# Kernel tuning notes

Hardware: AMD Instinct MI355X
Metric: run time of the kernel (lower is better)

Reference implementation:

```python
import jax, jax.numpy as jnp
import numpy as np

N = 100000
E = 1600000
IN_C, HID_C, OUT_C = 128, 64, 40


def setup_inputs() -> dict:
    key = jax.random.key(0)
    ks = jax.random.split(key, 9)
    x = jax.random.normal(ks[0], (N, IN_C), dtype=jnp.float32)
    src = jax.random.randint(ks[1], (E,), 0, N, dtype=jnp.int64)
    dst = jax.random.randint(ks[2], (E,), 0, N, dtype=jnp.int64)
    edge_index = jnp.stack([src, dst], axis=0)
    def glorot(k, fan_in, fan_out):
        s = jnp.sqrt(6.0 / (fan_in + fan_out)).astype(jnp.float32)
        return jax.random.uniform(k, (fan_in, fan_out), jnp.float32, -s, s)
    return {
        "x": x,
        "edge_index": edge_index,
        "W1": glorot(ks[3], IN_C, HID_C), "b1": jnp.zeros((HID_C,), jnp.float32),
        "W2": glorot(ks[4], HID_C, HID_C), "b2": jnp.zeros((HID_C,), jnp.float32),
        "W3": glorot(ks[5], HID_C, OUT_C), "b3": jnp.zeros((OUT_C,), jnp.float32),
    }


def _gcn_norm(edge_index, n_nodes):
    # add self-loops, then symmetric normalization D^-1/2 (A+I) D^-1/2
    loops = jnp.arange(n_nodes, dtype=edge_index.dtype)
    src = jnp.concatenate([edge_index[0], loops])
    dst = jnp.concatenate([edge_index[1], loops])
    deg = jax.ops.segment_sum(jnp.ones_like(dst, dtype=jnp.float32), dst,
                              num_segments=n_nodes)
    dinv = jnp.where(deg > 0, jax.lax.rsqrt(deg), 0.0)
    norm = dinv[src] * dinv[dst]  # [E + N]
    return src, dst, norm


def _gcn_conv(h, W, b, src, dst, norm, n_nodes):
    h = h @ W                                   # [N, out]
    msg = norm[:, None] * h[src]                # gather + scale, [E+N, out]
    out = jax.ops.segment_sum(msg, dst, num_segments=n_nodes)  # scatter-add
    return out + b


def reference(x, edge_index, W1, b1, W2, b2, W3, b3):
    n_nodes = x.shape[0]
    src, dst, norm = _gcn_norm(edge_index, n_nodes)
    h = jax.nn.relu(_gcn_conv(x, W1, b1, src, dst, norm, n_nodes))
    # dropout(p=0.5) is identity in eval mode
    h = jax.nn.relu(_gcn_conv(h, W2, b2, src, dst, norm, n_nodes))
    out = _gcn_conv(h, W3, b3, src, dst, norm, n_nodes)
    return out
```

## Files before the change

kernel.cpp:

```cpp
#include <hip/hip_runtime.h>

#define N_NODES 100000
#define N_EDGES 1600000
#define NBUCK 196
#define BCAP 9600
#define CH 4096
#define NCHUNK ((N_EDGES + CH - 1) / CH)

typedef __attribute__((ext_vector_type(2))) _Float16 half2v;
typedef __attribute__((ext_vector_type(4))) _Float16 half4v;
typedef __attribute__((ext_vector_type(8))) _Float16 half8v;
typedef __attribute__((ext_vector_type(4))) float f32x4;

__device__ __forceinline__ float4 loadX4(const float* X, size_t idx) {
    return *(const float4*)(X + idx);
}
__device__ __forceinline__ float4 loadX4(const _Float16* X, size_t idx) {
    half4v h = *(const half4v*)(X + idx);
    return make_float4((float)h.x, (float)h.y, (float)h.z, (float)h.w);
}


__global__ __launch_bounds__(256) void zero_small(int* p, int n) {
    int i = blockIdx.x * blockDim.x + threadIdx.x;
    if (i < n) p[i] = 0;
}

__global__ __launch_bounds__(256) void multisplit(const int* __restrict__ src,
                                                  const int* __restrict__ dst,
                                                  int* cursor,
                                                  int* __restrict__ bucketed, int e) {
    __shared__ int cnt[NBUCK];
    __shared__ int basel[NBUCK];
    const int t = threadIdx.x;
    const int base_e = blockIdx.x * CH;

    int myS[16], myD[16];
    for (int i = t; i < NBUCK; i += 256) cnt[i] = 0;
    __syncthreads();

#pragma unroll
    for (int k = 0; k < 16; ++k) {
        int i = base_e + k * 256 + t;
        if (i < e) {
            myS[k] = src[i];
            myD[k] = dst[i];
            atomicAdd(&cnt[myD[k] >> 9], 1);
        } else {
            myD[k] = -1;
        }
    }
    __syncthreads();
    for (int i = t; i < NBUCK; i += 256) basel[i] = atomicAdd(&cursor[i], cnt[i]);
    __syncthreads();
    for (int i = t; i < NBUCK; i += 256) cnt[i] = 0;
    __syncthreads();

#pragma unroll
    for (int k = 0; k < 16; ++k) {
        if (myD[k] >= 0) {
            int b = myD[k] >> 9;
            int pos = basel[b] + atomicAdd(&cnt[b], 1);
            if (pos < BCAP)
                bucketed[(size_t)b * BCAP + pos] = ((myD[k] & 511) << 17) | myS[k];
        }
    }
}

__global__ __launch_bounds__(256) void bucket_scan(const int* __restrict__ cursor,
                                                   int* __restrict__ gbase) {
    __shared__ int sm[256];
    const int t = threadIdx.x;
    int v = (t < NBUCK) ? cursor[t] : 0;
    sm[t] = v;
    __syncthreads();
    for (int off = 1; off < 256; off <<= 1) {
        int u = (t >= off) ? sm[t - off] : 0;
        __syncthreads();
        sm[t] += u;
        __syncthreads();
    }
    if (t < NBUCK) gbase[t] = sm[t] - v;
    if (t == NBUCK - 1) gbase[NBUCK] = sm[t];
}

__global__ __launch_bounds__(512) void build_csr(const int* __restrict__ bucketed,
                                                 const int* __restrict__ gbase,
                                                 int* __restrict__ row_ptr,
                                                 float* __restrict__ dinv,
                                                 int* __restrict__ csr_src, int n) {
    __shared__ int vals[BCAP];
    __shared__ int cnt[512];
    __shared__ int lcur[512];
    const int b = blockIdx.x;
    const int t = threadIdx.x;
    const int nb0 = b * 512;
    const int nn = min(512, n - nb0);
    const int gb = gbase[b];
    const int m = gbase[b + 1] - gb;

    cnt[t] = 0;
    __syncthreads();
    for (int i = t; i < m; i += 512) {
        int v = bucketed[(size_t)b * BCAP + i];
        vals[i] = v;
        atomicAdd(&cnt[v >> 17], 1);
    }
    __syncthreads();

    int deg = cnt[t];
    for (int off = 1; off < 512; off <<= 1) {
        int u = (t >= off) ? cnt[t - off] : 0;
        __syncthreads();
        cnt[t] += u;
        __syncthreads();
    }
    int offv = cnt[t] - deg;
    __syncthreads();
    cnt[t] = offv;
    lcur[t] = 0;
    if (t < nn) {
        row_ptr[nb0 + t] = gb + offv;
        dinv[nb0 + t] = rsqrtf((float)(deg + 1));
    }
    if (b == NBUCK - 1 && t == 0) row_ptr[n] = gb + m;
    __syncthreads();

    for (int i = t; i < m; i += 512) {
        int v = vals[i];
        int node = v >> 17;
        int pos = atomicAdd(&lcur[node], 1);
        csr_src[gb + cnt[node] + pos] = v & 0x1FFFF;
    }
}


template <int K>
__global__ __launch_bounds__(256) void transpose_w(const float* __restrict__ W,
                                                   _Float16* __restrict__ Wt) {
    int i = blockIdx.x * 256 + threadIdx.x;
    if (i < K * 64) {
        int k = i >> 6, nn = i & 63;
        Wt[(size_t)nn * K + k] = (_Float16)W[i];
    }
}


__device__ __forceinline__ void stageX_rows(const float* X, _Float16* Xl, int t,
                                            int row0, int n, int K, int SP) {
    for (int i = t; i < 64 * K / 4; i += 256) {
        int r = i / (K / 4), c = (i % (K / 4)) * 4;
        int grow = min(row0 + r, n - 1);
        float4 v = *(const float4*)(X + (size_t)grow * K + c);
        half4v h = {(_Float16)v.x, (_Float16)v.y, (_Float16)v.z, (_Float16)v.w};
        *(half4v*)(Xl + r * SP + c) = h;
    }
}
__device__ __forceinline__ void stageX_rows(const _Float16* X, _Float16* Xl, int t,
                                            int row0, int n, int K, int SP) {
    for (int i = t; i < 64 * K / 8; i += 256) {
        int r = i / (K / 8), c = (i % (K / 8)) * 8;
        int grow = min(row0 + r, n - 1);
        *(half8v*)(Xl + r * SP + c) = *(const half8v*)(X + (size_t)grow * K + c);
    }
}

template <int K, typename XT>
__global__ __launch_bounds__(256) void gemm_mfma64(const XT* __restrict__ X,
                                                   const _Float16* __restrict__ Wt,
                                                   const float* __restrict__ dinv,
                                                   _Float16* __restrict__ Y, int n) {
    constexpr int SP = K + 8;
    __shared__ _Float16 Xl[64 * SP];
    __shared__ _Float16 Wl[64 * SP];
    const int t = threadIdx.x;
    const int wave = t >> 6, lane = t & 63;
    const int row0 = blockIdx.x * 64;
    const int m = lane & 15, quad = lane >> 4;

    for (int i = t; i < 64 * K / 8; i += 256) {
        int r = i / (K / 8), c = (i % (K / 8)) * 8;
        *(half8v*)(Wl + r * SP + c) = *(const half8v*)(Wt + (size_t)r * K + c);
    }
    stageX_rows(X, Xl, t, row0, n, K, SP);
    __syncthreads();

    f32x4 acc[4] = {{0,0,0,0},{0,0,0,0},{0,0,0,0},{0,0,0,0}};
#pragma unroll
    for (int k0 = 0; k0 < K; k0 += 32) {
        half8v a = *(const half8v*)(Xl + (wave * 16 + m) * SP + k0 + quad * 8);
#pragma unroll
        for (int ct = 0; ct < 4; ++ct) {
            half8v b = *(const half8v*)(Wl + (ct * 16 + m) * SP + k0 + quad * 8);
            acc[ct] = __builtin_amdgcn_mfma_f32_16x16x32_f16(a, b, acc[ct], 0, 0, 0);
        }
    }

    float dv[4];
#pragma unroll
    for (int r = 0; r < 4; ++r) {
        int row = row0 + wave * 16 + quad * 4 + r;
        dv[r] = dinv[min(row, n - 1)];
    }
#pragma unroll
    for (int ct = 0; ct < 4; ++ct) {
#pragma unroll
        for (int r = 0; r < 4; ++r) {
            int row = row0 + wave * 16 + quad * 4 + r;
            if (row < n)
                Y[(size_t)row * 64 + ct * 16 + m] = (_Float16)(dv[r] * acc[ct][r]);
        }
    }
}


template <int K, int COUT, typename XT>
__global__ __launch_bounds__(256) void gemm_rt(const XT* __restrict__ X,
                                               const float* __restrict__ W,
                                               const float* __restrict__ dinv,
                                               _Float16* __restrict__ Y, int n) {
    constexpr int KC = 64;
    constexpr int S = KC + 4;
    constexpr int NCH = K / KC;
    __shared__ float Xl[64 * S];
    __shared__ float Wl[KC * COUT];

    const int t = threadIdx.x;
    const int row0 = blockIdx.x * 64;
    const int cg = (t & 15) * 4;
    const int rg = (t >> 4) * 4;

    float acc[4][4] = {};

#pragma unroll
    for (int ch = 0; ch < NCH; ++ch) {
        const int k0 = ch * KC;
        for (int i = t; i < 64 * KC / 4; i += 256) {
            int r = i >> 4;
            int k = (i & 15) * 4;
            int grow = min(row0 + r, n - 1);
            *(float4*)(Xl + r * S + k) = loadX4(X, (size_t)grow * K + k0 + k);
        }
        for (int i = t; i < KC * COUT / 4; i += 256) {
            *(float4*)(Wl + i * 4) = *(const float4*)(W + (size_t)k0 * COUT + (size_t)i * 4);
        }
        __syncthreads();

        if (cg < COUT) {
#pragma unroll 4
            for (int k = 0; k < KC; ++k) {
                float4 w = *(const float4*)(Wl + k * COUT + cg);
                float x0 = Xl[(rg + 0) * S + k];
                float x1 = Xl[(rg + 1) * S + k];
                float x2 = Xl[(rg + 2) * S + k];
                float x3 = Xl[(rg + 3) * S + k];
                acc[0][0] += x0 * w.x; acc[0][1] += x0 * w.y; acc[0][2] += x0 * w.z; acc[0][3] += x0 * w.w;
                acc[1][0] += x1 * w.x; acc[1][1] += x1 * w.y; acc[1][2] += x1 * w.z; acc[1][3] += x1 * w.w;
                acc[2][0] += x2 * w.x; acc[2][1] += x2 * w.y; acc[2][2] += x2 * w.z; acc[2][3] += x2 * w.w;
                acc[3][0] += x3 * w.x; acc[3][1] += x3 * w.y; acc[3][2] += x3 * w.z; acc[3][3] += x3 * w.w;
            }
        }
        __syncthreads();
    }

    if (cg < COUT) {
#pragma unroll
        for (int r = 0; r < 4; ++r) {
            int row = row0 + rg + r;
            if (row < n) {
                float d = dinv[row];
                half4v o = { (_Float16)(d * acc[r][0]), (_Float16)(d * acc[r][1]),
                             (_Float16)(d * acc[r][2]), (_Float16)(d * acc[r][3]) };
                *(half4v*)(Y + (size_t)row * COUT + cg) = o;
            }
        }
    }
}


template <bool RELU>
__global__ __launch_bounds__(256) void aggregate64b(const _Float16* __restrict__ tS,
                                                    const int* __restrict__ row_ptr,
                                                    const int* __restrict__ csr_src,
                                                    const float* __restrict__ dinv,
                                                    const float* __restrict__ bias,
                                                    _Float16* __restrict__ out, int n) {
    const int lane = threadIdx.x & 63;
    const int node = blockIdx.x * 4 + (threadIdx.x >> 6);
    if (node >= n) return;
    const int g = lane >> 3;
    const int c8 = lane & 7;
    const half8v* tS8 = (const half8v*)tS;

    const int beg = row_ptr[node];
    const int cnt = row_ptr[node + 1] - beg;

    half8v accA, accB;
#pragma unroll
    for (int i = 0; i < 8; ++i) { accA[i] = (_Float16)0; accB[i] = (_Float16)0; }

    for (int j0 = 0; j0 < cnt; j0 += 64) {
        const int m = min(64, cnt - j0);
        int sj = csr_src[beg + j0 + min(lane, m - 1)];

        int j = 0;
        for (; j + 16 <= m; j += 16) {
            int e0 = __shfl(sj, j + g);
            int e1 = __shfl(sj, j + 8 + g);
            half8v v0 = tS8[(size_t)e0 * 8 + c8];
            half8v v1 = tS8[(size_t)e1 * 8 + c8];
            accA += v0;
            accB += v1;
        }
        for (; j + 8 <= m; j += 8) {
            int e0 = __shfl(sj, j + g);
            accA += tS8[(size_t)e0 * 8 + c8];
        }
        if (j < m) {
            int idx = j + g;
            int e0 = __shfl(sj, min(idx, m - 1));
            half8v v = tS8[(size_t)e0 * 8 + c8];
            if (idx < m) accB += v;
        }
    }

    float acc[8];
#pragma unroll
    for (int i = 0; i < 8; ++i) acc[i] = (float)accA[i] + (float)accB[i];
#pragma unroll
    for (int off = 8; off < 64; off <<= 1) {
#pragma unroll
        for (int i = 0; i < 8; ++i) acc[i] += __shfl_xor(acc[i], off);
    }

    if (lane < 8) {
        half8v selfh = tS8[(size_t)node * 8 + c8];
        float4 b0 = *(const float4*)(bias + c8 * 8);
        float4 b1 = *(const float4*)(bias + c8 * 8 + 4);
        const float bb[8] = {b0.x, b0.y, b0.z, b0.w, b1.x, b1.y, b1.z, b1.w};
        float d = dinv[node];
        half8v o;
#pragma unroll
        for (int i = 0; i < 8; ++i) {
            float v = bb[i] + d * (acc[i] + (float)selfh[i]);
            if (RELU) v = fmaxf(v, 0.0f);
            o[i] = (_Float16)v;
        }
        ((half8v*)out)[(size_t)node * 8 + c8] = o;
    }
}


__global__ __launch_bounds__(256) void aggregate40v(const _Float16* __restrict__ tS,
                                                    const int* __restrict__ row_ptr,
                                                    const int* __restrict__ csr_src,
                                                    const float* __restrict__ dinv,
                                                    const float* __restrict__ bias,
                                                    float* __restrict__ out, int n) {
    const int lane = threadIdx.x & 63;
    const int node = blockIdx.x * 4 + (threadIdx.x >> 6);
    if (node >= n) return;
    const int g = lane / 20;
    const int c2 = lane - 20 * g;
    const bool act = (g < 3);
    const half2v* tS2 = (const half2v*)tS;

    const int beg = row_ptr[node];
    const int cnt = row_ptr[node + 1] - beg;

    half2v a0 = {(_Float16)0, (_Float16)0}, a1 = a0, a2 = a0, a3 = a0;

    for (int j0 = 0; j0 < cnt; j0 += 64) {
        const int m = min(64, cnt - j0);
        int sj = (lane < m) ? csr_src[beg + j0 + lane] : 0;

        int j = 0;
        for (; j + 12 <= m; j += 12) {
            int i0 = j + g, i1 = j + 3 + g, i2 = j + 6 + g, i3 = j + 9 + g;
            int e0 = __shfl(sj, i0 < m ? i0 : 0);
            int e1 = __shfl(sj, i1 < m ? i1 : 0);
            int e2 = __shfl(sj, i2 < m ? i2 : 0);
            int e3 = __shfl(sj, i3 < m ? i3 : 0);
            half2v v0 = tS2[(size_t)e0 * 20 + c2];
            half2v v1 = tS2[(size_t)e1 * 20 + c2];
            half2v v2 = tS2[(size_t)e2 * 20 + c2];
            half2v v3 = tS2[(size_t)e3 * 20 + c2];
            if (act) { a0 += v0; a1 += v1; a2 += v2; a3 += v3; }
        }
        for (; j + 3 <= m; j += 3) {
            int i0 = j + g;
            int e0 = __shfl(sj, i0 < m ? i0 : 0);
            half2v v0 = tS2[(size_t)e0 * 20 + c2];
            if (act) a0 += v0;
        }
        if (j < m) {
            int idx = j + g;
            int e0 = __shfl(sj, idx < m ? idx : m - 1);
            half2v v = tS2[(size_t)e0 * 20 + c2];
            if (act && idx < m) a1 += v;
        }
    }

    float2 s;
    s.x = ((float)a0.x + (float)a1.x) + ((float)a2.x + (float)a3.x);
    s.y = ((float)a0.y + (float)a1.y) + ((float)a2.y + (float)a3.y);
    float sx1 = __shfl(s.x, lane + 20), sy1 = __shfl(s.y, lane + 20);
    float sx2 = __shfl(s.x, lane + 40), sy2 = __shfl(s.y, lane + 40);
    if (lane < 20) {
        s.x += sx1 + sx2;
        s.y += sy1 + sy2;
        half2v selfh = tS2[(size_t)node * 20 + c2];
        float2 b = ((const float2*)bias)[c2];
        float d = dinv[node];
        float2 o;
        o.x = b.x + d * (s.x + (float)selfh.x);
        o.y = b.y + d * (s.y + (float)selfh.y);
        ((float2*)out)[(size_t)node * 20 + c2] = o;
    }
}


extern "C" void kernel_launch(void* const* d_in, const int* in_sizes, int n_in,
                              void* d_out, int out_size, void* d_ws, size_t ws_size,
                              hipStream_t stream) {
    const float* x  = (const float*)d_in[0];
    const int*   ei = (const int*)d_in[1];
    const int*   src = ei;
    const int*   dst = ei + N_EDGES;
    const float* W1 = (const float*)d_in[2];
    const float* b1 = (const float*)d_in[3];
    const float* W2 = (const float*)d_in[4];
    const float* b2 = (const float*)d_in[5];
    const float* W3 = (const float*)d_in[6];
    const float* b3 = (const float*)d_in[7];
    float* out = (float*)d_out;

    const int N = N_NODES, E = N_EDGES;

    char* p = (char*)d_ws;
    int*   cursor   = (int*)p;              p += 256 * 4;
    int*   gbase    = (int*)p;              p += 256 * 4;
    float* dinv     = (float*)p;            p += (size_t)N * 4;
    int*   row_ptr  = (int*)p;              p += (size_t)(N + 4) * 4;
    int*   bucketed = (int*)p;              p += (size_t)NBUCK * BCAP * 4;
    int*   csr_src  = (int*)p;              p += (size_t)E * 4;
    p = (char*)(((size_t)p + 15) & ~(size_t)15);
    _Float16* Wt1   = (_Float16*)p;         p += (size_t)64 * 128 * 2;
    _Float16* Wt2   = (_Float16*)p;         p += (size_t)64 * 64 * 2;
    _Float16* bufA  = (_Float16*)p;         p += (size_t)N * 64 * 2;
    p = (char*)(((size_t)p + 15) & ~(size_t)15);
    _Float16* bufB  = (_Float16*)p;         p += (size_t)N * 64 * 2;

    zero_small<<<1, 256, 0, stream>>>(cursor, NBUCK);
    transpose_w<128><<<32, 256, 0, stream>>>(W1, Wt1);
    transpose_w<64><<<16, 256, 0, stream>>>(W2, Wt2);
    multisplit<<<NCHUNK, 256, 0, stream>>>(src, dst, cursor, bucketed, E);
    bucket_scan<<<1, 256, 0, stream>>>(cursor, gbase);
    build_csr<<<NBUCK, 512, 0, stream>>>(bucketed, gbase, row_ptr, dinv, csr_src, N);

    const int aggGrid = (N + 3) / 4;
    const int gemmGrid = (N + 63) / 64;

    gemm_mfma64<128, float><<<gemmGrid, 256, 0, stream>>>(x, Wt1, dinv, bufA, N);
    aggregate64b<true><<<aggGrid, 256, 0, stream>>>(bufA, row_ptr, csr_src, dinv, b1, bufB, N);

    gemm_mfma64<64, _Float16><<<gemmGrid, 256, 0, stream>>>(bufB, Wt2, dinv, bufA, N);
    aggregate64b<true><<<aggGrid, 256, 0, stream>>>(bufA, row_ptr, csr_src, dinv, b2, bufB, N);

    gemm_rt<64, 40, _Float16><<<gemmGrid, 256, 0, stream>>>(bufB, W3, dinv, bufA, N);
    aggregate40v<<<aggGrid, 256, 0, stream>>>(bufA, row_ptr, csr_src, dinv, b3, out, N);
}
```

Baseline: 327.5 us.

## Assign one node per 8-lane group in aggregation and pad with a zero row

Both aggregation kernels are reworked so several nodes share a wavefront: 8 lanes per node for the 64-channel layers, and 10 lanes per node with 6 nodes per wave for the 40-channel layer. This replaces the one-wave-per-node scheme, which needed a cross-lane reduction and left most lanes idle on low-degree nodes. Out-of-range neighbor slots are redirected to an extra zeroed row at index n, which the GEMM kernels now write, so the gather loop needs no branches. In exchange, every node in a wave iterates up to the wave's largest degree, which costs work under degree skew. The 64-channel grid of N/32 assumes N is divisible by 32.

Result: faster. 311.3 us (-4.9%).

```diff
diff --git a/kernel.cpp b/kernel.cpp
--- a/kernel.cpp
+++ b/kernel.cpp
@@ -177,6 +177,8 @@
     const int wave = t >> 6, lane = t & 63;
     const int row0 = blockIdx.x * 64;
     const int m = lane & 15, quad = lane >> 4;
+
+    if (blockIdx.x == 0 && t < 32) ((int*)(Y + (size_t)n * 64))[t] = 0;
 
     for (int i = t; i < 64 * K / 8; i += 256) {
         int r = i / (K / 8), c = (i % (K / 8)) * 8;
@@ -229,6 +231,8 @@
     const int row0 = blockIdx.x * 64;
     const int cg = (t & 15) * 4;
     const int rg = (t >> 4) * 4;
+
+    if (blockIdx.x == 0 && t < COUT / 2) ((int*)(Y + (size_t)n * COUT))[t] = 0;
 
     float acc[4][4] = {};
 
@@ -279,143 +283,122 @@
 
 
 template <bool RELU>
-__global__ __launch_bounds__(256) void aggregate64b(const _Float16* __restrict__ tS,
+__global__ __launch_bounds__(256) void aggregate64c(const _Float16* __restrict__ tS,
                                                     const int* __restrict__ row_ptr,
                                                     const int* __restrict__ csr_src,
                                                     const float* __restrict__ dinv,
                                                     const float* __restrict__ bias,
                                                     _Float16* __restrict__ out, int n) {
-    const int lane = threadIdx.x & 63;
-    const int node = blockIdx.x * 4 + (threadIdx.x >> 6);
-    if (node >= n) return;
-    const int g = lane >> 3;
+    const int t = threadIdx.x;
+    const int lane = t & 63;
     const int c8 = lane & 7;
+    const int node = blockIdx.x * 32 + (t >> 3);
     const half8v* tS8 = (const half8v*)tS;
+    const int bpb = (lane & 56) << 2;
 
     const int beg = row_ptr[node];
     const int cnt = row_ptr[node + 1] - beg;
+    const int cl = (cnt > 0) ? cnt - 1 : 0;
+
+    int mc = cnt;
+    mc = max(mc, __shfl_xor(mc, 8));
+    mc = max(mc, __shfl_xor(mc, 16));
+    mc = max(mc, __shfl_xor(mc, 32));
 
     half8v accA, accB;
 #pragma unroll
     for (int i = 0; i < 8; ++i) { accA[i] = (_Float16)0; accB[i] = (_Float16)0; }
 
-    for (int j0 = 0; j0 < cnt; j0 += 64) {
-        const int m = min(64, cnt - j0);
-        int sj = csr_src[beg + j0 + min(lane, m - 1)];
-
-        int j = 0;
-        for (; j + 16 <= m; j += 16) {
-            int e0 = __shfl(sj, j + g);
-            int e1 = __shfl(sj, j + 8 + g);
-            half8v v0 = tS8[(size_t)e0 * 8 + c8];
-            half8v v1 = tS8[(size_t)e1 * 8 + c8];
-            accA += v0;
-            accB += v1;
-        }
-        for (; j + 8 <= m; j += 8) {
-            int e0 = __shfl(sj, j + g);
-            accA += tS8[(size_t)e0 * 8 + c8];
-        }
-        if (j < m) {
-            int idx = j + g;
-            int e0 = __shfl(sj, min(idx, m - 1));
-            half8v v = tS8[(size_t)e0 * 8 + c8];
-            if (idx < m) accB += v;
+    for (int j0 = 0; j0 < mc; j0 += 8) {
+        int sj = csr_src[beg + min(j0 + c8, cl)];
+#pragma unroll
+        for (int jj = 0; jj < 8; ++jj) {
+            int e = __builtin_amdgcn_ds_bpermute(bpb + jj * 4, sj);
+            e = (j0 + jj < cnt) ? e : n;
+            half8v v = tS8[(size_t)e * 8 + c8];
+            if (jj & 1) accB += v; else accA += v;
         }
     }
 
     float acc[8];
 #pragma unroll
     for (int i = 0; i < 8; ++i) acc[i] = (float)accA[i] + (float)accB[i];
-#pragma unroll
-    for (int off = 8; off < 64; off <<= 1) {
-#pragma unroll
-        for (int i = 0; i < 8; ++i) acc[i] += __shfl_xor(acc[i], off);
-    }
-
-    if (lane < 8) {
-        half8v selfh = tS8[(size_t)node * 8 + c8];
-        float4 b0 = *(const float4*)(bias + c8 * 8);
-        float4 b1 = *(const float4*)(bias + c8 * 8 + 4);
-        const float bb[8] = {b0.x, b0.y, b0.z, b0.w, b1.x, b1.y, b1.z, b1.w};
-        float d = dinv[node];
-        half8v o;
-#pragma unroll
-        for (int i = 0; i < 8; ++i) {
-            float v = bb[i] + d * (acc[i] + (float)selfh[i]);
-            if (RELU) v = fmaxf(v, 0.0f);
-            o[i] = (_Float16)v;
-        }
-        ((half8v*)out)[(size_t)node * 8 + c8] = o;
-    }
-}
-
-
-__global__ __launch_bounds__(256) void aggregate40v(const _Float16* __restrict__ tS,
+
+    half8v selfh = tS8[(size_t)node * 8 + c8];
+    float4 b0 = ((const float4*)bias)[c8 * 2];
+    float4 b1 = ((const float4*)bias)[c8 * 2 + 1];
+    const float bb[8] = {b0.x, b0.y, b0.z, b0.w, b1.x, b1.y, b1.z, b1.w};
+    float d = dinv[node];
+    half8v o;
+#pragma unroll
+    for (int i = 0; i < 8; ++i) {
+        float v = bb[i] + d * (acc[i] + (float)selfh[i]);
+        if (RELU) v = fmaxf(v, 0.0f);
+        o[i] = (_Float16)v;
+    }
+    ((half8v*)out)[(size_t)node * 8 + c8] = o;
+}
+
+
+__global__ __launch_bounds__(256) void aggregate40w(const _Float16* __restrict__ tS,
                                                     const int* __restrict__ row_ptr,
                                                     const int* __restrict__ csr_src,
                                                     const float* __restrict__ dinv,
                                                     const float* __restrict__ bias,
                                                     float* __restrict__ out, int n) {
-    const int lane = threadIdx.x & 63;
-    const int node = blockIdx.x * 4 + (threadIdx.x >> 6);
-    if (node >= n) return;
-    const int g = lane / 20;
-    const int c2 = lane - 20 * g;
-    const bool act = (g < 3);
-    const half2v* tS2 = (const half2v*)tS;
-
-    const int beg = row_ptr[node];
-    const int cnt = row_ptr[node + 1] - beg;
-
-    half2v a0 = {(_Float16)0, (_Float16)0}, a1 = a0, a2 = a0, a3 = a0;
-
-    for (int j0 = 0; j0 < cnt; j0 += 64) {
-        const int m = min(64, cnt - j0);
-        int sj = (lane < m) ? csr_src[beg + j0 + lane] : 0;
-
-        int j = 0;
-        for (; j + 12 <= m; j += 12) {
-            int i0 = j + g, i1 = j + 3 + g, i2 = j + 6 + g, i3 = j + 9 + g;
-            int e0 = __shfl(sj, i0 < m ? i0 : 0);
-            int e1 = __shfl(sj, i1 < m ? i1 : 0);
-            int e2 = __shfl(sj, i2 < m ? i2 : 0);
-            int e3 = __shfl(sj, i3 < m ? i3 : 0);
-            half2v v0 = tS2[(size_t)e0 * 20 + c2];
-            half2v v1 = tS2[(size_t)e1 * 20 + c2];
-            half2v v2 = tS2[(size_t)e2 * 20 + c2];
-            half2v v3 = tS2[(size_t)e3 * 20 + c2];
-            if (act) { a0 += v0; a1 += v1; a2 += v2; a3 += v3; }
-        }
-        for (; j + 3 <= m; j += 3) {
-            int i0 = j + g;
-            int e0 = __shfl(sj, i0 < m ? i0 : 0);
-            half2v v0 = tS2[(size_t)e0 * 20 + c2];
-            if (act) a0 += v0;
-        }
-        if (j < m) {
-            int idx = j + g;
-            int e0 = __shfl(sj, idx < m ? idx : m - 1);
-            half2v v = tS2[(size_t)e0 * 20 + c2];
-            if (act && idx < m) a1 += v;
-        }
-    }
-
-    float2 s;
-    s.x = ((float)a0.x + (float)a1.x) + ((float)a2.x + (float)a3.x);
-    s.y = ((float)a0.y + (float)a1.y) + ((float)a2.y + (float)a3.y);
-    float sx1 = __shfl(s.x, lane + 20), sy1 = __shfl(s.y, lane + 20);
-    float sx2 = __shfl(s.x, lane + 40), sy2 = __shfl(s.y, lane + 40);
-    if (lane < 20) {
-        s.x += sx1 + sx2;
-        s.y += sy1 + sy2;
-        half2v selfh = tS2[(size_t)node * 20 + c2];
-        float2 b = ((const float2*)bias)[c2];
+    const int t = threadIdx.x;
+    const int lane = t & 63;
+    const int wave = t >> 6;
+    const int g = lane / 10;
+    const int c10 = lane - g * 10;
+    const int node = blockIdx.x * 24 + wave * 6 + g;
+    const bool act = (g < 6) && (node < n);
+    const half4v* tS4 = (const half4v*)tS;
+    const int bpb = g * 40;
+
+    const int nclamp = act ? node : 0;
+    const int beg = row_ptr[nclamp];
+    const int cnt = act ? (row_ptr[nclamp + 1] - beg) : 0;
+    const int cl = (cnt > 0) ? cnt - 1 : 0;
+
+    int mc = cnt;
+    mc = max(mc, __shfl_xor(mc, 1));
+    mc = max(mc, __shfl_xor(mc, 2));
+    mc = max(mc, __shfl_xor(mc, 4));
+    mc = max(mc, __shfl_xor(mc, 8));
+    mc = max(mc, __shfl_xor(mc, 16));
+    mc = max(mc, __shfl_xor(mc, 32));
+
+    half4v accA, accB;
+#pragma unroll
+    for (int i = 0; i < 4; ++i) { accA[i] = (_Float16)0; accB[i] = (_Float16)0; }
+
+    for (int j0 = 0; j0 < mc; j0 += 10) {
+        int sj = csr_src[beg + min(j0 + c10, cl)];
+#pragma unroll
+        for (int jj = 0; jj < 10; ++jj) {
+            int e = __builtin_amdgcn_ds_bpermute(bpb + jj * 4, sj);
+            e = (j0 + jj < cnt) ? e : n;
+            half4v v = tS4[(size_t)e * 10 + c10];
+            if (jj & 1) accB += v; else accA += v;
+        }
+    }
+
+    if (act) {
+        float acc[4];
+#pragma unroll
+        for (int i = 0; i < 4; ++i) acc[i] = (float)accA[i] + (float)accB[i];
+
+        half4v selfh = tS4[(size_t)node * 10 + c10];
+        float4 b = ((const float4*)bias)[c10];
+        const float bb[4] = {b.x, b.y, b.z, b.w};
         float d = dinv[node];
-        float2 o;
-        o.x = b.x + d * (s.x + (float)selfh.x);
-        o.y = b.y + d * (s.y + (float)selfh.y);
-        ((float2*)out)[(size_t)node * 20 + c2] = o;
+        float4 o;
+        o.x = bb[0] + d * (acc[0] + (float)selfh[0]);
+        o.y = bb[1] + d * (acc[1] + (float)selfh[1]);
+        o.z = bb[2] + d * (acc[2] + (float)selfh[2]);
+        o.w = bb[3] + d * (acc[3] + (float)selfh[3]);
+        *(float4*)(out + (size_t)node * 40 + c10 * 4) = o;
     }
 }
 
@@ -447,7 +430,7 @@
     p = (char*)(((size_t)p + 15) & ~(size_t)15);
     _Float16* Wt1   = (_Float16*)p;         p += (size_t)64 * 128 * 2;
     _Float16* Wt2   = (_Float16*)p;         p += (size_t)64 * 64 * 2;
-    _Float16* bufA  = (_Float16*)p;         p += (size_t)N * 64 * 2;
+    _Float16* bufA  = (_Float16*)p;         p += (size_t)(N + 64) * 64 * 2;
     p = (char*)(((size_t)p + 15) & ~(size_t)15);
     _Float16* bufB  = (_Float16*)p;         p += (size_t)N * 64 * 2;
 
@@ -458,15 +441,16 @@
     bucket_scan<<<1, 256, 0, stream>>>(cursor, gbase);
     build_csr<<<NBUCK, 512, 0, stream>>>(bucketed, gbase, row_ptr, dinv, csr_src, N);
 
-    const int aggGrid = (N + 3) / 4;
+    const int agg64Grid = N / 32;
+    const int agg40Grid = (N + 23) / 24;
     const int gemmGrid = (N + 63) / 64;
 
     gemm_mfma64<128, float><<<gemmGrid, 256, 0, stream>>>(x, Wt1, dinv, bufA, N);
-    aggregate64b<true><<<aggGrid, 256, 0, stream>>>(bufA, row_ptr, csr_src, dinv, b1, bufB, N);
+    aggregate64c<true><<<agg64Grid, 256, 0, stream>>>(bufA, row_ptr, csr_src, dinv, b1, bufB, N);
 
     gemm_mfma64<64, _Float16><<<gemmGrid, 256, 0, stream>>>(bufB, Wt2, dinv, bufA, N);
-    aggregate64b<true><<<aggGrid, 256, 0, stream>>>(bufA, row_ptr, csr_src, dinv, b2, bufB, N);
+    aggregate64c<true><<<agg64Grid, 256, 0, stream>>>(bufA, row_ptr, csr_src, dinv, b2, bufB, N);
 
     gemm_rt<64, 40, _Float16><<<gemmGrid, 256, 0, stream>>>(bufB, W3, dinv, bufA, N);
-    aggregate40v<<<aggGrid, 256, 0, stream>>>(bufA, row_ptr, csr_src, dinv, b3, out, N);
-}
+    aggregate40w<<<agg40Grid, 256, 0, stream>>>(bufA, row_ptr, csr_src, dinv, b3, out, N);
+}
```
